# Performance work log

Measured on AMD Instinct MI355X. Metric: run time of the kernel, lower is better.

The kernel has to match this reference:

```python
import jax, jax.numpy as jnp
import numpy as np


def leaky(x):
    return jnp.where(x > 0, x, 0.2 * x)


def conv(x, w, b, s, p):
    y = jax.lax.conv_general_dilated(x, w, (s, s), [(p, p), (p, p)],
                                     dimension_numbers=('NCHW', 'OIHW', 'NCHW'))
    return y + b[None, :, None, None]


def maxpool2s1(x):
    return jax.lax.reduce_window(x, -jnp.inf, jax.lax.max, (1, 1, 2, 2), (1, 1, 1, 1), 'VALID')


def bn_eval(x, g, b, m, v):
    scale = g / jnp.sqrt(v + 1e-5)
    return (x - m[None, :, None, None]) * scale[None, :, None, None] + b[None, :, None, None]


def adaptive_avg_pool(x, oh, ow):
    # matches torch AdaptiveAvgPool2d window rule: [floor(i*H/o), ceil((i+1)*H/o))
    B, C, H, W = x.shape
    rows = []
    for i in range(oh):
        hs, he = (i * H) // oh, -((-(i + 1) * H) // oh)
        cols = []
        for j in range(ow):
            ws, we = (j * W) // ow, -((-(j + 1) * W) // ow)
            cols.append(x[:, :, hs:he, ws:we].mean((2, 3)))
        rows.append(jnp.stack(cols, -1))
    return jnp.stack(rows, -2)  # [B,C,oh,ow]


def forward(x, tw1, tb1, tw2, tb2, tw3, tb3, tw4, tb4,
            sw1, sb1, bn1_g, bn1_b, bn1_m, bn1_v,
            sw2, sb2, bn2_g, bn2_b, bn2_m, bn2_v,
            cw, cb, ew1, eb1, ew2, eb2, ew3, eb3):
    B = x.shape[0]
    E, K = ew1.shape[0], 2
    # --- scout router (BN in eval mode with running stats) ---
    h = jax.nn.relu(bn_eval(conv(x, sw1, sb1, 4, 3), bn1_g, bn1_b, bn1_m, bn1_v))
    h = jax.nn.relu(bn_eval(conv(h, sw2, sb2, 2, 1), bn2_g, bn2_b, bn2_m, bn2_v))
    logits = h.mean((2, 3)) @ cw.T + cb                       # [B,E]
    gate = jax.nn.softmax(logits, axis=-1)
    topk_p, topk_i = jax.lax.top_k(gate, K)                   # [B,K]
    topk_p = topk_p / (topk_p.sum(-1, keepdims=True) + 1e-6)
    # --- shared trunk ---
    t = maxpool2s1(leaky(conv(x, tw1, tb1, 4, 1)))            # 224->56->55
    t = maxpool2s1(leaky(conv(t, tw2, tb2, 2, 2)))            # 55->28->27
    t = leaky(conv(t, tw3, tb3, 1, 1))                        # 27
    t = maxpool2s1(leaky(conv(t, tw4, tb4, 1, 1)))            # 27->26
    t = adaptive_avg_pool(t, 3, 3)                            # [B,128,3,3]
    flat = t.reshape(B, -1)                                   # [B,1152]
    # --- MoE head: dense per-expert MLP, masked weighted combine ---
    h1 = leaky(jnp.einsum('bi,eoi->beo', flat, ew1) + eb1[None])   # [B,E,1024]
    h2 = leaky(jnp.einsum('beh,eoh->beo', h1, ew2) + eb2[None])    # [B,E,512]
    h3 = jnp.einsum('beh,eoh->beo', h2, ew3) + eb3[None]           # [B,E,feat]
    onehot = (topk_i[:, :, None] == jnp.arange(E)[None, None, :])  # [B,K,E]
    comb_w = jnp.sum(topk_p[:, :, None] * onehot, axis=1)          # [B,E]
    out = jnp.einsum('beo,be->bo', h3, comb_w)                     # [B,feat]
    return out


def setup_inputs() -> dict:
    key = jax.random.key(0)
    ks = jax.random.split(key, 32)
    W = 0.02
    d = {}
    d['x'] = jax.random.normal(ks[0], (256, 3, 224, 224), jnp.float32)
    d['tw1'] = jax.random.normal(ks[1], (16, 3, 3, 3), jnp.float32) * W
    d['tb1'] = jnp.zeros((16,), jnp.float32)
    d['tw2'] = jax.random.normal(ks[2], (32, 16, 5, 5), jnp.float32) * W
    d['tb2'] = jnp.zeros((32,), jnp.float32)
    d['tw3'] = jax.random.normal(ks[3], (64, 32, 3, 3), jnp.float32) * W
    d['tb3'] = jnp.zeros((64,), jnp.float32)
    d['tw4'] = jax.random.normal(ks[4], (128, 64, 3, 3), jnp.float32) * W
    d['tb4'] = jnp.zeros((128,), jnp.float32)
    d['sw1'] = jax.random.normal(ks[5], (16, 3, 7, 7), jnp.float32) * W
    d['sb1'] = jnp.zeros((16,), jnp.float32)
    d['bn1_g'] = jnp.ones((16,), jnp.float32)
    d['bn1_b'] = jnp.zeros((16,), jnp.float32)
    d['bn1_m'] = jnp.zeros((16,), jnp.float32)
    d['bn1_v'] = jnp.ones((16,), jnp.float32)
    d['sw2'] = jax.random.normal(ks[6], (32, 16, 3, 3), jnp.float32) * W
    d['sb2'] = jnp.zeros((32,), jnp.float32)
    d['bn2_g'] = jnp.ones((32,), jnp.float32)
    d['bn2_b'] = jnp.zeros((32,), jnp.float32)
    d['bn2_m'] = jnp.zeros((32,), jnp.float32)
    d['bn2_v'] = jnp.ones((32,), jnp.float32)
    d['cw'] = jax.random.normal(ks[7], (3, 32), jnp.float32) * W
    d['cb'] = jnp.zeros((3,), jnp.float32)
    d['ew1'] = jax.random.normal(ks[8], (3, 1024, 1152), jnp.float32) * W
    d['eb1'] = jnp.zeros((3, 1024), jnp.float32)
    d['ew2'] = jax.random.normal(ks[9], (3, 512, 1024), jnp.float32) * W
    d['eb2'] = jnp.zeros((3, 512), jnp.float32)
    d['ew3'] = jax.random.normal(ks[10], (3, 512, 512), jnp.float32) * W
    d['eb3'] = jnp.zeros((3, 512), jnp.float32)
    return d


def reference(x, tw1, tb1, tw2, tb2, tw3, tb3, tw4, tb4,
              sw1, sb1, bn1_g, bn1_b, bn1_m, bn1_v,
              sw2, sb2, bn2_g, bn2_b, bn2_m, bn2_v,
              cw, cb, ew1, eb1, ew2, eb2, ew3, eb3):
    return forward(x, tw1, tb1, tw2, tb2, tw3, tb3, tw4, tb4,
                   sw1, sb1, bn1_g, bn1_b, bn1_m, bn1_v,
                   sw2, sb2, bn2_g, bn2_b, bn2_m, bn2_v,
                   cw, cb, ew1, eb1, ew2, eb2, ew3, eb3)
```

## Files before the change

### kernel.cpp

```cpp
#include <hip/hip_runtime.h>

#define DEV static __device__ __forceinline__

constexpr int BATCH = 256;

DEV float leakyf(float x){ return x > 0.f ? x : 0.2f * x; }

typedef _Float16 f16x8 __attribute__((ext_vector_type(8)));
typedef float f32x4 __attribute__((ext_vector_type(4)));

template<int IC,int OC>
__global__ __launch_bounds__(256) void wpackM_k(const float* __restrict__ w,
    _Float16* __restrict__ wp){
  constexpr int S = IC/32, F = OC/16;
  int i = blockIdx.x*256 + threadIdx.x;
  if (i >= 9*S*F*512) return;
  int j = i & 7, L = (i >> 3) & 63, rest = i >> 9;
  int f = rest % F; int q2 = rest / F; int s = q2 % S; int t = q2 / S;
  int oc = f*16 + (L & 15), ic = s*32 + (L >> 4)*8 + j;
  wp[i] = (_Float16)w[((size_t)oc*IC + ic)*9 + t];
}

template<int OC,int K>
__global__ __launch_bounds__(256) void wpackS_k(const float* __restrict__ w,
    _Float16* __restrict__ wp){
  constexpr int F = OC/16, KWP = (K+1)/2;
  int i = blockIdx.x*256 + threadIdx.x;
  if (i >= K*KWP*F*512) return;
  int j = i & 7, L = (i >> 3) & 63, rest = i >> 9;
  int f = rest % F, s = rest / F;
  int kh = s / KWP, kwp = s % KWP;
  int k = (L >> 4)*8 + j;
  int kw = 2*kwp + (k >> 4), ic = k & 15;
  int oc = f*16 + (L & 15);
  float v = (kw < K) ? w[((size_t)(oc*16 + ic)*K + kh)*K + kw] : 0.f;
  wp[i] = (_Float16)v;
}

__global__ __launch_bounds__(256) void wpackF_k(const float* __restrict__ sw1,
    const float* __restrict__ tw1, _Float16* __restrict__ wp){
  int i = blockIdx.x*256 + threadIdx.x;
  if (i >= 6*2*512) return;
  int j = i & 7, L = (i >> 3) & 63, rest = i >> 9;
  int nf = rest & 1, s = rest >> 1;
  int k = s*32 + (L >> 4)*8 + j;
  int oc = L & 15;
  int t = k / 48, c = k % 48;
  int dr = (t >> 1) - 1, dc = (t & 1) - 1;
  int ic = c >> 4, pr = (c >> 2) & 3, pc = c & 3;
  float v = 0.f;
  if (nf == 0){
    int kh = 4*dr + pr + 3, kw = 4*dc + pc + 3;
    if (kh >= 0 && kh < 7 && kw >= 0 && kw < 7) v = sw1[((oc*3 + ic)*7 + kh)*7 + kw];
  } else {
    int kh = 4*dr + pr + 1, kw = 4*dc + pc + 1;
    if (kh >= 0 && kh < 3 && kw >= 0 && kw < 3) v = tw1[((oc*3 + ic)*3 + kh)*3 + kw];
  }
  wp[i] = (_Float16)v;
}

template<int KTOT>
__global__ __launch_bounds__(256) void wpackGh_k(const float* __restrict__ w, int N,
    _Float16* __restrict__ wp){
  const int NF = N >> 4, KT = KTOT >> 5;
  const int total = NF * KT * 512;
  const int e = blockIdx.y;
  w  += (size_t)e * N * KTOT;
  wp += (size_t)e * total;
  int i = blockIdx.x*256 + threadIdx.x;
  if (i >= total) return;
  int j = i & 7, L = (i >> 3) & 63, rest = i >> 9;
  int nf = rest % NF, t = rest / NF;
  int n = nf*16 + (L & 15), k = t*32 + (L >> 4)*8 + j;
  wp[i] = (_Float16)w[(size_t)n*KTOT + k];
}

__global__ __launch_bounds__(256) void acvt_k(const float* __restrict__ in,
    _Float16* __restrict__ o16, int nelem){
  int i = blockIdx.x*256 + threadIdx.x;
  if (i >= nelem) return;
  o16[i] = (_Float16)in[i];
}

__global__ __launch_bounds__(256) void fusedM_k(
    const float* __restrict__ x,
    const _Float16* __restrict__ W,
    const float* __restrict__ sb, const float* __restrict__ cb_,
    const float* __restrict__ g, const float* __restrict__ bt,
    const float* __restrict__ mn, const float* __restrict__ vr,
    _Float16* __restrict__ s1out, _Float16* __restrict__ c1out){
  __shared__ __align__(16) _Float16 Ah[3*58*64];
  const int tid = threadIdx.x;
  const int n = blockIdx.x / 28, oh0 = (blockIdx.x % 28) * 2;

  if (tid < 48){
    int rr = tid >> 4, side = (tid >> 3) & 1, q = tid & 7;
    int col = side ? 57 : 0;
    *(int4*)((char*)Ah + (((rr*58 + col) << 7) + q*16)) = (int4){0,0,0,0};
  }

  {
    const int m = tid & 63;
    const bool mok = (m < 56);
    const int cc = m + 1;
    int rc0 = tid >> 6;
    int ic   = (rc0 == 3) ? 0 : rc0;
    int ridx = (rc0 == 3) ? 1 : 0;
    #pragma unroll
    for (int j = 0; j < 9; ++j){
      const int ih = 4*oh0 - 4 + ridx;
      if (mok){
        float4 v = {0.f,0.f,0.f,0.f};
        if (ih >= 0)
          v = *(const float4*)(x + ((size_t)(n*3 + ic)*224 + ih)*224 + 4*m);
        const int rr = ridx >> 2, pr = ridx & 3;
        int boff = (((rr*58 + cc) << 7) + ic*32 + pr*8) ^ ((cc & 7) << 4);
        _Float16 h4[4] = {(_Float16)v.x, (_Float16)v.y, (_Float16)v.z, (_Float16)v.w};
        *(unsigned long long*)((char*)Ah + boff) = *(unsigned long long*)h4;
      }
      ic += 1; ridx += 1;
      if (ic >= 3){ ic -= 3; ridx += 1; }
    }
  }
  __syncthreads();

  const int wid = tid >> 6, lane = tid & 63;
  const int kg8 = (lane >> 4) * 8;
  f32x4 acc[2][2];
  #pragma unroll
  for (int mi = 0; mi < 2; ++mi)
    #pragma unroll
    for (int nf = 0; nf < 2; ++nf) acc[mi][nf] = (f32x4){0.f,0.f,0.f,0.f};

  #pragma unroll
  for (int s = 0; s < 6; ++s){
    const int kk = s*32 + kg8;
    const int t = kk / 48, c0 = kk - t*48;
    const int ra = t >> 1, ca = t & 1;
    f16x8 ah[2];
    #pragma unroll
    for (int mi = 0; mi < 2; ++mi){
      const int m = 2*wid + mi;
      const int rowsel = m >> 2;
      const int ow = (m & 3)*16 + (lane & 15);
      const int owc = ow > 55 ? 55 : ow;
      const int col = owc + ca;
      const int bidx = ((((rowsel + ra)*58 + col) << 7) + c0*2) ^ ((col & 7) << 4);
      ah[mi] = *(const f16x8*)((const char*)Ah + bidx);
    }
    #pragma unroll
    for (int nf = 0; nf < 2; ++nf){
      const f16x8 bw = *(const f16x8*)(W + (s*2 + nf)*512 + lane*8);
      #pragma unroll
      for (int mi = 0; mi < 2; ++mi)
        acc[mi][nf] = __builtin_amdgcn_mfma_f32_16x16x32_f16(ah[mi], bw, acc[mi][nf], 0,0,0);
    }
  }

  const int oc = lane & 15;
  const float sbv = sb[oc];
  const float scv = g[oc] * __frsqrt_rn(vr[oc] + 1e-5f);
  const float mnv = mn[oc], btv = bt[oc], cbv = cb_[oc];
  #pragma unroll
  for (int mi = 0; mi < 2; ++mi){
    const int m = 2*wid + mi;
    const int row = oh0 + (m >> 2);
    const int owb = (m & 3)*16 + (lane >> 4)*4;
    #pragma unroll
    for (int r = 0; r < 4; ++r){
      const int ow = owb + r;
      if (ow >= 56) continue;
      float vs = acc[mi][0][r] + sbv;
      vs = fmaxf((vs - mnv)*scv + btv, 0.f);
      const size_t o = (((size_t)n*56 + row)*56 + ow)*16 + oc;
      s1out[o] = (_Float16)vs;
      c1out[o] = (_Float16)leakyf(acc[mi][1][r] + cbv);
    }
  }
}

template<int OC,int K,int P,int IH,int IW,int ACT,bool OUT16,bool GATE>
__global__ __launch_bounds__(256) void convS_k(
    const _Float16* __restrict__ in,
    const _Float16* __restrict__ W,
    const float* __restrict__ bias,
    const float* __restrict__ bng, const float* __restrict__ bnb,
    const float* __restrict__ bnm, const float* __restrict__ bnv,
    float* __restrict__ outF, _Float16* __restrict__ outH,
    float* __restrict__ gsum){
  constexpr int F = OC/16, KWP = (K+1)/2;
  __shared__ __align__(16) _Float16 A[K*60*16];
  __shared__ float gred[32];

  const int tid = threadIdx.x;
  const int n = blockIdx.x / 28, oh = blockIdx.x % 28;

  if (GATE && tid < 32) gred[tid] = 0.f;

  for (int i = tid; i < K*60*2; i += 256){
    int half = i & 1; int p = i >> 1;
    int c = p % 60; int r = p / 60;
    int ih = 2*oh - P + r, iw = c - P;
    int4 v = {0,0,0,0};
    if (ih >= 0 && ih < IH && iw >= 0 && iw < IW)
      v = *(const int4*)(in + (((size_t)n*IH + ih)*IW + iw)*16 + half*8);
    int byte = ((r*60 + c)*32 + half*16) ^ (((c>>1)&7) << 4);
    *(int4*)((char*)A + byte) = v;
  }
  __syncthreads();

  const int wid = tid >> 6, lane = tid & 63;
  const int fsel = wid & 1, mb = wid >> 1;
  const int ow_l = min(mb*16 + (lane & 15), 27);
  const int ic0b = ((lane >> 4) & 1) * 16;
  const int kwo  = (lane >> 4) >> 1;

  f32x4 acc = {0.f,0.f,0.f,0.f};
  #pragma unroll
  for (int kh = 0; kh < K; ++kh){
    #pragma unroll
    for (int kwp = 0; kwp < KWP; ++kwp){
      const int kw = 2*kwp + kwo;
      const int c = 2*ow_l + kw;
      int byte = ((kh*60 + c)*32 + ic0b) ^ (((c>>1)&7) << 4);
      f16x8 a = *(const f16x8*)((const char*)A + byte);
      const int s = kh*KWP + kwp;
      const f16x8 b = *(const f16x8*)(W + (s*F + fsel)*512 + lane*8);
      acc = __builtin_amdgcn_mfma_f32_16x16x32_f16(a, b, acc, 0,0,0);
    }
  }

  const int oc = fsel*16 + (lane & 15);
  float bv = bias[oc], sc = 1.f, mm = 0.f, bb = 0.f;
  if (ACT == 1){
    sc = bng[oc] * __frsqrt_rn(bnv[oc] + 1e-5f);
    mm = bnm[oc]; bb = bnb[oc];
  }
  float lsum = 0.f;
  #pragma unroll
  for (int r = 0; r < 4; ++r){
    const int ow = mb*16 + (lane >> 4)*4 + r;
    if (ow >= 28) continue;
    float v = acc[r] + bv;
    if (ACT == 1) v = fmaxf((v - mm)*sc + bb, 0.f);
    else          v = leakyf(v);
    if (GATE){
      lsum += v;
    } else {
      const size_t o = (((size_t)n*28 + oh)*28 + ow)*OC + oc;
      if (OUT16) outH[o] = (_Float16)v;
      else       outF[o] = v;
    }
  }
  if (GATE){
    atomicAdd(&gred[oc], lsum);
    __syncthreads();
    if (tid < 32) atomicAdd(&gsum[n*32 + tid], gred[tid]);
  }
}

template<int IC,int OC,int OUTM>
__global__ __launch_bounds__(256) void convM_k(
    const _Float16* __restrict__ Ag,
    const _Float16* __restrict__ W,
    const float* __restrict__ bias,
    _Float16* __restrict__ OutPad, _Float16* __restrict__ OutNP)
{
  constexpr int S = IC/32, FTOT = OC/16, FW = FTOT/2;
  constexpr int ICB = IC*2, ICG = ICB/16;
  __shared__ __align__(16) char A[4*34*ICB];

  const int tid = threadIdx.x;
  const int bx = blockIdx.x;
  const int n = bx / 14, pr = bx % 14;
  const int oh0 = pr * 2;

  const size_t gbase = ((size_t)n*29) * 29 * IC;
  for (int g = tid; g < 4*34*ICG; g += 256){
    int r = g / (34*ICG);
    int rem = g - r*(34*ICG);
    int c = rem / ICG, q = rem - c*ICG;
    int rp = oh0 + r;
    int4 v = {0,0,0,0};
    if (rp <= 28 && c < 29){
      size_t e = gbase + ((size_t)rp*29 + c)*IC + q*8;
      v = *(const int4*)(Ag + e);
    }
    int off = (r*34 + c)*ICB + q*16;
    int swz = off ^ ((c & 7) << 4);
    *(int4*)(A + swz) = v;
  }
  __syncthreads();

  const int wid = tid >> 6, lane = tid & 63;
  const int rsel = wid & 1, ocq = wid >> 1;
  const int c0 = lane & 15, kg = (lane >> 4) * 16;
  const int colb0 = c0*ICB + kg, colb1 = (16 + c0)*ICB + kg;
  int msk[3];
  #pragma unroll
  for (int kw = 0; kw < 3; ++kw) msk[kw] = ((c0 + kw) & 7) << 4;

  f32x4 acc[2][FW];
  #pragma unroll
  for (int m = 0; m < 2; ++m)
    #pragma unroll
    for (int f = 0; f < FW; ++f) acc[m][f] = (f32x4){0.f,0.f,0.f,0.f};

  #pragma unroll
  for (int kh = 0; kh < 3; ++kh){
    #pragma unroll
    for (int kw = 0; kw < 3; ++kw){
      #pragma unroll
      for (int s = 0; s < S; ++s){
        const int fr0 = (((kh*3 + kw)*S + s)*FTOT + ocq*FW) * 512 + lane*8;
        f16x8 b[FW];
        #pragma unroll
        for (int f = 0; f < FW; ++f)
          b[f] = *(const f16x8*)(W + fr0 + f*512);
        const int base = ((rsel + kh)*34 + kw)*ICB + s*64;
        const int o0 = (base + colb0) ^ msk[kw];
        const int o1 = (base + colb1) ^ msk[kw];
        f16x8 a0 = *(const f16x8*)(A + o0);
        f16x8 a1 = *(const f16x8*)(A + o1);
        #pragma unroll
        for (int f = 0; f < FW; ++f){
          acc[0][f] = __builtin_amdgcn_mfma_f32_16x16x32_f16(a0, b[f], acc[0][f], 0,0,0);
          acc[1][f] = __builtin_amdgcn_mfma_f32_16x16x32_f16(a1, b[f], acc[1][f], 0,0,0);
        }
      }
    }
  }

  const int orow = oh0 + rsel;
  if (orow >= 27) return;
  #pragma unroll
  for (int f = 0; f < FW; ++f){
    const int oc = (ocq*FW + f)*16 + c0;
    const float bv = bias[oc];
    #pragma unroll
    for (int m = 0; m < 2; ++m){
      #pragma unroll
      for (int r = 0; r < 4; ++r){
        const int ow = m*16 + (lane >> 4)*4 + r;
        if (ow >= 27) continue;
        float v = leakyf(acc[m][f][r] + bv);
        if (OUTM == 0){
          OutPad[(((size_t)n*29 + orow+1)*29 + ow+1)*OC + oc] = (_Float16)v;
        } else {
          OutNP[(((size_t)n*27 + orow)*27 + ow)*OC + oc] = (_Float16)v;
        }
      }
    }
  }
}

template<int KTOT,int ACT,int OUTM>
__global__ __launch_bounds__(256) void gemmH_k(
    const _Float16* __restrict__ A, long strideA,
    const _Float16* __restrict__ W,
    const float* __restrict__ bias, int N,
    _Float16* __restrict__ OutH, float* __restrict__ OutF){
  const int e = blockIdx.z;
  A += (size_t)e * strideA;
  const int NF = N >> 4, KT = KTOT >> 5;
  W += (size_t)e * NF * KT * 512;
  const float* bs = bias + (size_t)e * N;
  const size_t ob = (size_t)e * 256 * N;

  const int tid = threadIdx.x, wid = tid >> 6, lane = tid & 63;
  const int mblk = blockIdx.x * 32;
  const int nf = blockIdx.y * 4 + wid;
  const int r0 = mblk + (lane & 15);
  const int kof = (lane >> 4) * 8;

  f32x4 acc0 = {0,0,0,0}, acc1 = {0,0,0,0};
  for (int t = 0; t < KT; ++t){
    const int k = t*32 + kof;
    f16x8 a0 = *(const f16x8*)(A + (size_t)r0*KTOT + k);
    f16x8 a1 = *(const f16x8*)(A + (size_t)(r0+16)*KTOT + k);
    const f16x8 b = *(const f16x8*)(W + ((size_t)t*NF + nf)*512 + lane*8);
    acc0 = __builtin_amdgcn_mfma_f32_16x16x32_f16(a0, b, acc0, 0,0,0);
    acc1 = __builtin_amdgcn_mfma_f32_16x16x32_f16(a1, b, acc1, 0,0,0);
  }
  const int n = nf*16 + (lane & 15);
  const float bv = bs[n];
  #pragma unroll
  for (int mi = 0; mi < 2; ++mi){
    f32x4 a = mi ? acc1 : acc0;
    #pragma unroll
    for (int r = 0; r < 4; ++r){
      const int m = mblk + mi*16 + (lane >> 4)*4 + r;
      float v = a[r] + bv;
      if (ACT == 1) v = leakyf(v);
      const size_t o = ob + (size_t)m*N + n;
      if (OUTM == 0) OutH[o] = (_Float16)v;
      else           OutF[o] = v;
    }
  }
}

__global__ __launch_bounds__(256) void poolh_k(const _Float16* __restrict__ in,
                                               _Float16* __restrict__ out){
  int idx = blockIdx.x * 256 + threadIdx.x;
  if (idx >= BATCH * 55 * 55 * 2) return;
  int half = idx & 1; int p = idx >> 1;
  int ow = p % 55; int t = p / 55; int oh = t % 55; int n = t / 55;
  const _Float16* q = in + (((size_t)n*56 + oh)*56 + ow)*16 + half*8;
  f16x8 a = *(const f16x8*)q;
  f16x8 b = *(const f16x8*)(q + 16);
  f16x8 c = *(const f16x8*)(q + 56*16);
  f16x8 d = *(const f16x8*)(q + 57*16);
  f16x8 r;
  #pragma unroll
  for (int j = 0; j < 8; ++j){
    float m = fmaxf(fmaxf((float)a[j], (float)b[j]), fmaxf((float)c[j], (float)d[j]));
    r[j] = (_Float16)m;
  }
  *(f16x8*)(out + (size_t)p*16 + half*8) = r;
}

__global__ __launch_bounds__(256) void pool2n_k(const _Float16* __restrict__ in,
    _Float16* __restrict__ o16){
  int idx = blockIdx.x*256 + threadIdx.x;
  if (idx >= BATCH*27*27*32) return;
  int ic = idx & 31; int p = idx >> 5;
  int ow = p % 27; int t = p / 27; int oh = t % 27; int n = t / 27;
  const _Float16* b = in + (((size_t)n*28 + oh)*28 + ow)*32 + ic;
  float v = fmaxf(fmaxf((float)b[0], (float)b[32]),
                  fmaxf((float)b[28*32], (float)b[29*32]));
  o16[(((size_t)n*29 + oh+1)*29 + ow+1)*32 + ic] = (_Float16)v;
}

__global__ __launch_bounds__(256) void gate2_k(const float* __restrict__ gsum,
                                               const float* __restrict__ cw,
                                               const float* __restrict__ cb,
                                               float* __restrict__ comb){
  int n = blockIdx.x * 256 + threadIdx.x;
  if (n >= BATCH) return;
  float mch[32];
  #pragma unroll
  for (int c = 0; c < 32; ++c) mch[c] = gsum[n*32 + c] / 784.f;
  float lg[3];
  #pragma unroll
  for (int e = 0; e < 3; ++e){
    float a = cb[e];
    #pragma unroll
    for (int c = 0; c < 32; ++c) a += mch[c] * cw[e*32 + c];
    lg[e] = a;
  }
  float m = fmaxf(lg[0], fmaxf(lg[1], lg[2]));
  float ex[3], sum = 0.f;
  #pragma unroll
  for (int e = 0; e < 3; ++e){ ex[e] = expf(lg[e] - m); sum += ex[e]; }
  float pr[3];
  #pragma unroll
  for (int e = 0; e < 3; ++e) pr[e] = ex[e] / sum;
  int i1 = 0;
  if (pr[1] > pr[0]) i1 = 1;
  if (pr[2] > pr[i1]) i1 = 2;
  int i2 = -1;
  for (int e = 0; e < 3; ++e){
    if (e == i1) continue;
    if (i2 < 0 || pr[e] > pr[i2]) i2 = e;
  }
  float s12 = pr[i1] + pr[i2] + 1e-6f;
  float cmb[3] = {0.f, 0.f, 0.f};
  cmb[i1] = pr[i1] / s12;
  cmb[i2] = pr[i2] / s12;
  comb[n*3 + 0] = cmb[0];
  comb[n*3 + 1] = cmb[1];
  comb[n*3 + 2] = cmb[2];
}

__global__ __launch_bounds__(256) void papool2_k(const _Float16* __restrict__ in,
                                                 float* __restrict__ flat){
  __shared__ float red[2][128][9];
  const int n = blockIdx.x;
  const int tid = threadIdx.x;
  const int h = tid >> 7, c = tid & 127;
  const _Float16* p = in + (size_t)n * 729 * 128 + c;

  float sum[9];
  #pragma unroll
  for (int j = 0; j < 9; ++j) sum[j] = 0.f;

  float prev[27], cur[27];
  const int r0 = h * 13;
  #pragma unroll
  for (int rr = 0; rr < 14; ++rr){
    const int r = r0 + rr;
    #pragma unroll
    for (int cc = 0; cc < 27; ++cc)
      cur[cc] = (float)p[(size_t)(r*27 + cc) * 128];
    if (rr > 0){
      const int pr = r - 1;
      const bool b0 = (pr < 9), b1 = (pr >= 8) && (pr < 18), b2 = (pr >= 17);
      #pragma unroll
      for (int cc = 0; cc < 26; ++cc){
        float v = fmaxf(fmaxf(prev[cc], prev[cc+1]), fmaxf(cur[cc], cur[cc+1]));
        if (b0){
          if (cc < 9)             sum[0] += v;
          if (cc >= 8 && cc < 18) sum[1] += v;
          if (cc >= 17)           sum[2] += v;
        }
        if (b1){
          if (cc < 9)             sum[3] += v;
          if (cc >= 8 && cc < 18) sum[4] += v;
          if (cc >= 17)           sum[5] += v;
        }
        if (b2){
          if (cc < 9)             sum[6] += v;
          if (cc >= 8 && cc < 18) sum[7] += v;
          if (cc >= 17)           sum[8] += v;
        }
      }
    }
    #pragma unroll
    for (int cc = 0; cc < 27; ++cc) prev[cc] = cur[cc];
  }

  #pragma unroll
  for (int j = 0; j < 9; ++j) red[h][c][j] = sum[j];
  __syncthreads();

  if (tid < 128){
    const float rcp[9] = {1.f/81, 1.f/90, 1.f/81, 1.f/90, 1.f/100, 1.f/90,
                          1.f/81, 1.f/90, 1.f/81};
    float* o = flat + (size_t)n * 1152 + tid * 9;
    #pragma unroll
    for (int j = 0; j < 9; ++j)
      o[j] = (red[0][tid][j] + red[1][tid][j]) * rcp[j];
  }
}

__global__ __launch_bounds__(256) void comb_k(const float* __restrict__ h3,
                                              const float* __restrict__ comb,
                                              float* __restrict__ out){
  int idx = blockIdx.x * 256 + threadIdx.x;
  if (idx >= BATCH * 512) return;
  int o = idx % 512, b = idx / 512;
  float s = 0.f;
  #pragma unroll
  for (int e = 0; e < 3; ++e)
    s += comb[b * 3 + e] * h3[((size_t)e * BATCH + b) * 512 + o];
  out[idx] = s;
}

extern "C" void kernel_launch(void* const* d_in, const int* in_sizes, int n_in,
                              void* d_out, int out_size, void* d_ws, size_t ws_size,
                              hipStream_t stream){
  const float* x    = (const float*)d_in[0];
  const float* tw1  = (const float*)d_in[1];  const float* tb1 = (const float*)d_in[2];
  const float* tw2  = (const float*)d_in[3];  const float* tb2 = (const float*)d_in[4];
  const float* tw3  = (const float*)d_in[5];  const float* tb3 = (const float*)d_in[6];
  const float* tw4  = (const float*)d_in[7];  const float* tb4 = (const float*)d_in[8];
  const float* sw1  = (const float*)d_in[9];  const float* sb1 = (const float*)d_in[10];
  const float* bn1g = (const float*)d_in[11]; const float* bn1b = (const float*)d_in[12];
  const float* bn1m = (const float*)d_in[13]; const float* bn1v = (const float*)d_in[14];
  const float* sw2  = (const float*)d_in[15]; const float* sb2 = (const float*)d_in[16];
  const float* bn2g = (const float*)d_in[17]; const float* bn2b = (const float*)d_in[18];
  const float* bn2m = (const float*)d_in[19]; const float* bn2v = (const float*)d_in[20];
  const float* cw   = (const float*)d_in[21]; const float* cb  = (const float*)d_in[22];
  const float* ew1  = (const float*)d_in[23]; const float* eb1 = (const float*)d_in[24];
  const float* ew2  = (const float*)d_in[25]; const float* eb2 = (const float*)d_in[26];
  const float* ew3  = (const float*)d_in[27]; const float* eb3 = (const float*)d_in[28];
  float* out = (float*)d_out;

  float* ws = (float*)d_ws;
  size_t off = 0;
  float* comb   = ws + off; off += 768;
  float* flat   = ws + off; off += (size_t)BATCH * 1152;
  float* h3     = ws + off; off += (size_t)BATCH * 3 * 512;
  float* gsum   = ws + off; off += BATCH * 32;
  _Float16* wpk3 = (_Float16*)(ws + off); off += 9216;
  _Float16* wpk4 = (_Float16*)(ws + off); off += 36864;
  _Float16* wp2  = (_Float16*)(ws + off); off += 7680;
  _Float16* wps2 = (_Float16*)(ws + off); off += 3072;
  _Float16* wpf  = (_Float16*)(ws + off); off += 3072;
  off += 16;
  float* bufA   = ws + off; off += 13778944;
  off += 16;
  float* bufB   = ws + off; off += 23887872;
  off += 16;
  (void)ws_size; (void)in_sizes; (void)n_in; (void)out_size;

  _Float16* s1h = (_Float16*)bufA;
  _Float16* c1h = (_Float16*)bufB;
  _Float16* p1h = (_Float16*)bufA;
  _Float16* c2h = (_Float16*)bufB;
  _Float16* P2 = (_Float16*)(bufB + 8000000);
  _Float16* C3 = (_Float16*)bufA;
  _Float16* c4h = (_Float16*)bufB;

  _Float16* hb = (_Float16*)bufB;
  size_t uo = 0;
  _Float16* ewp1 = hb + uo; uo += 3538944;
  _Float16* ewp2 = hb + uo; uo += 1572864;
  _Float16* ewp3 = hb + uo; uo += 786432;
  _Float16* f16a = hb + uo; uo += 294912;
  _Float16* h1   = hb + uo; uo += 786432;
  _Float16* h2   = hb + uo; uo += 393216;

  dim3 blk(256);

  hipMemsetAsync(gsum, 0, BATCH * 32 * sizeof(float), stream);
  wpackM_k<32,64>  <<<dim3(72),  blk, 0, stream>>>(tw3, wpk3);
  wpackM_k<64,128> <<<dim3(288), blk, 0, stream>>>(tw4, wpk4);
  wpackS_k<32,5><<<dim3(60), blk, 0, stream>>>(tw2, wp2);
  wpackS_k<32,3><<<dim3(24), blk, 0, stream>>>(sw2, wps2);
  wpackF_k<<<dim3(24), blk, 0, stream>>>(sw1, tw1, wpf);

  fusedM_k<<<dim3(BATCH*28), blk, 0, stream>>>(
      x, wpf, sb1, tb1, bn1g, bn1b, bn1m, bn1v, s1h, c1h);

  convS_k<32,3,1,56,56,1,false,true><<<dim3(BATCH*28), blk, 0, stream>>>(
      s1h, wps2, sb2, bn2g, bn2b, bn2m, bn2v, nullptr, nullptr, gsum);
  gate2_k<<<dim3(1), blk, 0, stream>>>(gsum, cw, cb, comb);

  poolh_k<<<dim3((BATCH*55*55*2 + 255)/256), blk, 0, stream>>>(c1h, p1h);
  convS_k<32,5,2,55,55,0,true,false><<<dim3(BATCH*28), blk, 0, stream>>>(
      p1h, wp2, tb2, nullptr, nullptr, nullptr, nullptr, nullptr, c2h, nullptr);

  hipMemsetAsync(P2, 0, (size_t)6889472 * 2, stream);
  pool2n_k<<<dim3((BATCH*27*27*32 + 255)/256), blk, 0, stream>>>(c2h, P2);

  hipMemsetAsync(C3, 0, (size_t)13778944 * 2, stream);
  convM_k<32,64,0><<<dim3(BATCH*14), blk, 0, stream>>>(
      P2, wpk3, tb3, C3, nullptr);

  convM_k<64,128,1><<<dim3(BATCH*14), blk, 0, stream>>>(
      C3, wpk4, tb4, nullptr, c4h);

  papool2_k<<<dim3(BATCH), blk, 0, stream>>>(c4h, flat);

  wpackGh_k<1152><<<dim3(4608,3), blk, 0, stream>>>(ew1, 1024, ewp1);
  wpackGh_k<1024><<<dim3(2048,3), blk, 0, stream>>>(ew2,  512, ewp2);
  wpackGh_k< 512><<<dim3(1024,3), blk, 0, stream>>>(ew3,  512, ewp3);
  acvt_k<<<dim3(1152), blk, 0, stream>>>(flat, f16a, BATCH*1152);

  gemmH_k<1152,1,0><<<dim3(8,16,3), blk, 0, stream>>>(
      f16a, 0L, ewp1, eb1, 1024, h1, nullptr);
  gemmH_k<1024,1,0><<<dim3(8,8,3), blk, 0, stream>>>(
      h1, 256L*1024, ewp2, eb2, 512, h2, nullptr);
  gemmH_k< 512,0,1><<<dim3(8,8,3), blk, 0, stream>>>(
      h2, 256L*512, ewp3, eb3, 512, nullptr, h3);

  comb_k<<<dim3(512), blk, 0, stream>>>(h3, comb, out);
}
```

Before: 303.7 us.

## Fuse maxpool layers into following conv input loads and drop padded buffers

Measured after the change: 275.8 us. -9.2%, faster.

```diff
diff --git a/kernel.cpp b/kernel.cpp
--- a/kernel.cpp
+++ b/kernel.cpp
@@ -8,6 +8,13 @@
 
 typedef _Float16 f16x8 __attribute__((ext_vector_type(8)));
 typedef float f32x4 __attribute__((ext_vector_type(4)));
+
+DEV f16x8 max8(f16x8 a, f16x8 b){
+  f16x8 r;
+  #pragma unroll
+  for (int j = 0; j < 8; ++j) r[j] = a[j] > b[j] ? a[j] : b[j];
+  return r;
+}
 
 template<int IC,int OC>
 __global__ __launch_bounds__(256) void wpackM_k(const float* __restrict__ w,
@@ -179,7 +186,7 @@
   }
 }
 
-template<int OC,int K,int P,int IH,int IW,int ACT,bool OUT16,bool GATE>
+template<int OC,int K,int P,int IH,int IW,int ACT,bool OUT16,bool GATE,bool POOLIN>
 __global__ __launch_bounds__(256) void convS_k(
     const _Float16* __restrict__ in,
     const _Float16* __restrict__ W,
@@ -189,6 +196,7 @@
     float* __restrict__ outF, _Float16* __restrict__ outH,
     float* __restrict__ gsum){
   constexpr int F = OC/16, KWP = (K+1)/2;
+  constexpr int RW = POOLIN ? (IW+1) : IW;
   __shared__ __align__(16) _Float16 A[K*60*16];
   __shared__ float gred[32];
 
@@ -202,8 +210,19 @@
     int c = p % 60; int r = p / 60;
     int ih = 2*oh - P + r, iw = c - P;
     int4 v = {0,0,0,0};
-    if (ih >= 0 && ih < IH && iw >= 0 && iw < IW)
-      v = *(const int4*)(in + (((size_t)n*IH + ih)*IW + iw)*16 + half*8);
+    if (ih >= 0 && ih < IH && iw >= 0 && iw < IW){
+      const _Float16* q = in + (((size_t)n*(POOLIN ? IH+1 : IH) + ih)*RW + iw)*16 + half*8;
+      if (POOLIN){
+        f16x8 a = *(const f16x8*)q;
+        f16x8 b = *(const f16x8*)(q + 16);
+        f16x8 cc = *(const f16x8*)(q + RW*16);
+        f16x8 d = *(const f16x8*)(q + RW*16 + 16);
+        f16x8 mx = max8(max8(a, b), max8(cc, d));
+        v = *(int4*)&mx;
+      } else {
+        v = *(const int4*)q;
+      }
+    }
     int byte = ((r*60 + c)*32 + half*16) ^ (((c>>1)&7) << 4);
     *(int4*)((char*)A + byte) = v;
   }
@@ -259,12 +278,12 @@
   }
 }
 
-template<int IC,int OC,int OUTM>
+template<int IC,int OC,bool POOLIN>
 __global__ __launch_bounds__(256) void convM_k(
     const _Float16* __restrict__ Ag,
     const _Float16* __restrict__ W,
     const float* __restrict__ bias,
-    _Float16* __restrict__ OutPad, _Float16* __restrict__ OutNP)
+    _Float16* __restrict__ Out)
 {
   constexpr int S = IC/32, FTOT = OC/16, FW = FTOT/2;
   constexpr int ICB = IC*2, ICG = ICB/16;
@@ -275,16 +294,24 @@
   const int n = bx / 14, pr = bx % 14;
   const int oh0 = pr * 2;
 
-  const size_t gbase = ((size_t)n*29) * 29 * IC;
   for (int g = tid; g < 4*34*ICG; g += 256){
     int r = g / (34*ICG);
     int rem = g - r*(34*ICG);
     int c = rem / ICG, q = rem - c*ICG;
-    int rp = oh0 + r;
+    int ir = oh0 + r - 1, icol = c - 1;
     int4 v = {0,0,0,0};
-    if (rp <= 28 && c < 29){
-      size_t e = gbase + ((size_t)rp*29 + c)*IC + q*8;
-      v = *(const int4*)(Ag + e);
+    if (ir >= 0 && ir < 27 && icol >= 0 && icol < 27){
+      if (POOLIN){
+        const _Float16* p0 = Ag + (((size_t)n*28 + ir)*28 + icol)*IC + q*8;
+        f16x8 a = *(const f16x8*)p0;
+        f16x8 b = *(const f16x8*)(p0 + IC);
+        f16x8 cc = *(const f16x8*)(p0 + 28*IC);
+        f16x8 d = *(const f16x8*)(p0 + 28*IC + IC);
+        f16x8 mx = max8(max8(a, b), max8(cc, d));
+        v = *(int4*)&mx;
+      } else {
+        v = *(const int4*)(Ag + (((size_t)n*27 + ir)*27 + icol)*IC + q*8);
+      }
     }
     int off = (r*34 + c)*ICB + q*16;
     int swz = off ^ ((c & 7) << 4);
@@ -344,11 +371,7 @@
         const int ow = m*16 + (lane >> 4)*4 + r;
         if (ow >= 27) continue;
         float v = leakyf(acc[m][f][r] + bv);
-        if (OUTM == 0){
-          OutPad[(((size_t)n*29 + orow+1)*29 + ow+1)*OC + oc] = (_Float16)v;
-        } else {
-          OutNP[(((size_t)n*27 + orow)*27 + ow)*OC + oc] = (_Float16)v;
-        }
+        Out[(((size_t)n*27 + orow)*27 + ow)*OC + oc] = (_Float16)v;
       }
     }
   }
@@ -397,38 +420,6 @@
       else           OutF[o] = v;
     }
   }
-}
-
-__global__ __launch_bounds__(256) void poolh_k(const _Float16* __restrict__ in,
-                                               _Float16* __restrict__ out){
-  int idx = blockIdx.x * 256 + threadIdx.x;
-  if (idx >= BATCH * 55 * 55 * 2) return;
-  int half = idx & 1; int p = idx >> 1;
-  int ow = p % 55; int t = p / 55; int oh = t % 55; int n = t / 55;
-  const _Float16* q = in + (((size_t)n*56 + oh)*56 + ow)*16 + half*8;
-  f16x8 a = *(const f16x8*)q;
-  f16x8 b = *(const f16x8*)(q + 16);
-  f16x8 c = *(const f16x8*)(q + 56*16);
-  f16x8 d = *(const f16x8*)(q + 57*16);
-  f16x8 r;
-  #pragma unroll
-  for (int j = 0; j < 8; ++j){
-    float m = fmaxf(fmaxf((float)a[j], (float)b[j]), fmaxf((float)c[j], (float)d[j]));
-    r[j] = (_Float16)m;
-  }
-  *(f16x8*)(out + (size_t)p*16 + half*8) = r;
-}
-
-__global__ __launch_bounds__(256) void pool2n_k(const _Float16* __restrict__ in,
-    _Float16* __restrict__ o16){
-  int idx = blockIdx.x*256 + threadIdx.x;
-  if (idx >= BATCH*27*27*32) return;
-  int ic = idx & 31; int p = idx >> 5;
-  int ow = p % 27; int t = p / 27; int oh = t % 27; int n = t / 27;
-  const _Float16* b = in + (((size_t)n*28 + oh)*28 + ow)*32 + ic;
-  float v = fmaxf(fmaxf((float)b[0], (float)b[32]),
-                  fmaxf((float)b[28*32], (float)b[29*32]));
-  o16[(((size_t)n*29 + oh+1)*29 + ow+1)*32 + ic] = (_Float16)v;
 }
 
 __global__ __launch_bounds__(256) void gate2_k(const float* __restrict__ gsum,
@@ -586,10 +577,8 @@
 
   _Float16* s1h = (_Float16*)bufA;
   _Float16* c1h = (_Float16*)bufB;
-  _Float16* p1h = (_Float16*)bufA;
-  _Float16* c2h = (_Float16*)bufB;
-  _Float16* P2 = (_Float16*)(bufB + 8000000);
-  _Float16* C3 = (_Float16*)bufA;
+  _Float16* c2h = (_Float16*)(bufB + 14000000);
+  _Float16* C3u = (_Float16*)bufA;
   _Float16* c4h = (_Float16*)bufB;
 
   _Float16* hb = (_Float16*)bufB;
@@ -613,23 +602,18 @@
   fusedM_k<<<dim3(BATCH*28), blk, 0, stream>>>(
       x, wpf, sb1, tb1, bn1g, bn1b, bn1m, bn1v, s1h, c1h);
 
-  convS_k<32,3,1,56,56,1,false,true><<<dim3(BATCH*28), blk, 0, stream>>>(
+  convS_k<32,3,1,56,56,1,false,true,false><<<dim3(BATCH*28), blk, 0, stream>>>(
       s1h, wps2, sb2, bn2g, bn2b, bn2m, bn2v, nullptr, nullptr, gsum);
   gate2_k<<<dim3(1), blk, 0, stream>>>(gsum, cw, cb, comb);
 
-  poolh_k<<<dim3((BATCH*55*55*2 + 255)/256), blk, 0, stream>>>(c1h, p1h);
-  convS_k<32,5,2,55,55,0,true,false><<<dim3(BATCH*28), blk, 0, stream>>>(
-      p1h, wp2, tb2, nullptr, nullptr, nullptr, nullptr, nullptr, c2h, nullptr);
-
-  hipMemsetAsync(P2, 0, (size_t)6889472 * 2, stream);
-  pool2n_k<<<dim3((BATCH*27*27*32 + 255)/256), blk, 0, stream>>>(c2h, P2);
-
-  hipMemsetAsync(C3, 0, (size_t)13778944 * 2, stream);
-  convM_k<32,64,0><<<dim3(BATCH*14), blk, 0, stream>>>(
-      P2, wpk3, tb3, C3, nullptr);
-
-  convM_k<64,128,1><<<dim3(BATCH*14), blk, 0, stream>>>(
-      C3, wpk4, tb4, nullptr, c4h);
+  convS_k<32,5,2,55,55,0,true,false,true><<<dim3(BATCH*28), blk, 0, stream>>>(
+      c1h, wp2, tb2, nullptr, nullptr, nullptr, nullptr, nullptr, c2h, nullptr);
+
+  convM_k<32,64,true><<<dim3(BATCH*14), blk, 0, stream>>>(
+      c2h, wpk3, tb3, C3u);
+
+  convM_k<64,128,false><<<dim3(BATCH*14), blk, 0, stream>>>(
+      C3u, wpk4, tb4, c4h);
 
   papool2_k<<<dim3(BATCH), blk, 0, stream>>>(c4h, flat);
 
```
